# Optimization experiments

Measured on AMD Instinct MI355X. Metric: run time of the kernel, lower is better.

Reference implementation:

```python
import jax, jax.numpy as jnp
import numpy as np

E = 768
H_HEADS = 12


def trilinear_border_sample(feat_map, coords):
    """grid_sample 3D, mode='bilinear', padding_mode='border', align_corners=True.
    feat_map: (B, C, D, H, W); coords: (B, P, 3) in [-1,1], last dim = (x, y, z) -> (W, H, D).
    Returns (B, P, C).
    """
    B, C, D, H, W = feat_map.shape
    x, y, z = coords[..., 0], coords[..., 1], coords[..., 2]
    ix = (x + 1.0) * 0.5 * (W - 1)
    iy = (y + 1.0) * 0.5 * (H - 1)
    iz = (z + 1.0) * 0.5 * (D - 1)
    x0 = jnp.floor(ix); y0 = jnp.floor(iy); z0 = jnp.floor(iz)
    wx = ix - x0; wy = iy - y0; wz = iz - z0
    x0i = jnp.clip(x0, 0, W - 1).astype(jnp.int32)
    x1i = jnp.clip(x0 + 1, 0, W - 1).astype(jnp.int32)
    y0i = jnp.clip(y0, 0, H - 1).astype(jnp.int32)
    y1i = jnp.clip(y0 + 1, 0, H - 1).astype(jnp.int32)
    z0i = jnp.clip(z0, 0, D - 1).astype(jnp.int32)
    z1i = jnp.clip(z0 + 1, 0, D - 1).astype(jnp.int32)
    flat = feat_map.reshape(B, C, D * H * W)

    def gather(zi, yi, xi):
        idx = (zi * H + yi) * W + xi  # (B, P)
        return jnp.take_along_axis(flat, idx[:, None, :], axis=2)  # (B, C, P)

    out = (
        gather(z0i, y0i, x0i) * ((1 - wz) * (1 - wy) * (1 - wx))[:, None, :]
        + gather(z0i, y0i, x1i) * ((1 - wz) * (1 - wy) * wx)[:, None, :]
        + gather(z0i, y1i, x0i) * ((1 - wz) * wy * (1 - wx))[:, None, :]
        + gather(z0i, y1i, x1i) * ((1 - wz) * wy * wx)[:, None, :]
        + gather(z1i, y0i, x0i) * (wz * (1 - wy) * (1 - wx))[:, None, :]
        + gather(z1i, y0i, x1i) * (wz * (1 - wy) * wx)[:, None, :]
        + gather(z1i, y1i, x0i) * (wz * wy * (1 - wx))[:, None, :]
        + gather(z1i, y1i, x1i) * (wz * wy * wx)[:, None, :]
    )
    return out.transpose(0, 2, 1)  # (B, P, C)


def setup_inputs() -> dict:
    key = jax.random.key(0)
    ks = jax.random.split(key, 12)
    B, fullN, nb = 64, 513, 32
    s = 1.0 / np.sqrt(E)
    return {
        "x": jax.random.normal(ks[0], (B, fullN, E), jnp.float32),
        "bio_embed": jax.random.normal(ks[1], (B, E), jnp.float32),
        "base_coords": jax.random.uniform(ks[2], (nb, 3), jnp.float32),
        "offsets": jax.random.normal(ks[3], (B, nb, 3), jnp.float32) * 0.1,
        "confidence": jax.random.uniform(ks[4], (B, 1), jnp.float32),
        "sample_proj_w": jax.random.uniform(ks[5], (E, E), jnp.float32, -s, s),
        "sample_proj_b": jax.random.uniform(ks[6], (E,), jnp.float32, -s, s),
        "in_proj_w": jax.random.uniform(ks[7], (3 * E, E), jnp.float32, -s, s),
        "in_proj_b": jnp.zeros((3 * E,), jnp.float32),
        "out_proj_w": jax.random.uniform(ks[8], (E, E), jnp.float32, -s, s),
        "out_proj_b": jnp.zeros((E,), jnp.float32),
        "grid_size": 8,
    }


def reference(x, bio_embed, base_coords, offsets, confidence,
              sample_proj_w, sample_proj_b, in_proj_w, in_proj_b,
              out_proj_w, out_proj_b, grid_size):
    B, fullN, C = x.shape
    G = grid_size
    patch_tokens = x[:, 1:, :]  # (B, N, C), N = G^3
    feat_map = patch_tokens.transpose(0, 2, 1).reshape(B, C, G, G, G)

    coords = jnp.clip(base_coords[None, :, :] + offsets, -1.0, 1.0)  # (B, nb, 3)
    sampled = trilinear_border_sample(feat_map, coords)  # (B, nb, C)
    sampled = sampled @ sample_proj_w.T + sample_proj_b

    # MultiheadAttention: single query (bio_embed), keys/values = sampled tokens
    hd = E // H_HEADS
    Wq, Wk, Wv = in_proj_w[:E], in_proj_w[E:2 * E], in_proj_w[2 * E:]
    bq, bk, bv = in_proj_b[:E], in_proj_b[E:2 * E], in_proj_b[2 * E:]
    q = (bio_embed @ Wq.T + bq).reshape(B, H_HEADS, hd)
    k = (sampled @ Wk.T + bk).reshape(B, -1, H_HEADS, hd)
    v = (sampled @ Wv.T + bv).reshape(B, -1, H_HEADS, hd)
    scores = jnp.einsum('bhd,bphd->bhp', q, k) / jnp.sqrt(jnp.asarray(hd, q.dtype))
    attn = jax.nn.softmax(scores, axis=-1)
    ctx = jnp.einsum('bhp,bphd->bhd', attn, v).reshape(B, E)
    attn_out = ctx @ out_proj_w.T + out_proj_b  # (B, E)

    out = jnp.broadcast_to(attn_out[:, None, :], (B, fullN, C))
    out = out * confidence[:, :, None]
    return out
```

## Files before the change

kernel.cpp:

```cpp
#include <hip/hip_runtime.h>
#include <hip/hip_bf16.h>
#include <math.h>

#define E 768
#define NH 12
#define HD 64
#define NTHR 256

typedef __attribute__((ext_vector_type(8))) short bf16x8;
typedef __attribute__((ext_vector_type(4))) float f32x4;

__device__ __forceinline__ unsigned short f2bf_rne(float f) {
    unsigned int u = __float_as_uint(f);
    u += 0x7FFF + ((u >> 16) & 1);
    return (unsigned short)(u >> 16);
}

__device__ __forceinline__ float bf2f(unsigned short u) {
    return __uint_as_float((unsigned)u << 16);
}

__device__ __forceinline__ void sample_one(
    const float* x, const float* bcrd, const float* offs, int G,
    unsigned short* sampled, int u, int P, int fullN, int t, int tstep)
{
    int b = u / P, p = u % P;
    float gm1 = (float)(G - 1);

    float cx = bcrd[p * 3 + 0] + offs[u * 3 + 0];
    float cy = bcrd[p * 3 + 1] + offs[u * 3 + 1];
    float cz = bcrd[p * 3 + 2] + offs[u * 3 + 2];
    cx = fminf(fmaxf(cx, -1.f), 1.f);
    cy = fminf(fmaxf(cy, -1.f), 1.f);
    cz = fminf(fmaxf(cz, -1.f), 1.f);

    float ix = (cx + 1.f) * 0.5f * gm1;
    float iy = (cy + 1.f) * 0.5f * gm1;
    float iz = (cz + 1.f) * 0.5f * gm1;
    float fx = floorf(ix), fy = floorf(iy), fz = floorf(iz);
    float wx = ix - fx, wy = iy - fy, wz = iz - fz;

    int x0 = (int)fminf(fmaxf(fx,       0.f), gm1);
    int x1 = (int)fminf(fmaxf(fx + 1.f, 0.f), gm1);
    int y0 = (int)fminf(fmaxf(fy,       0.f), gm1);
    int y1 = (int)fminf(fmaxf(fy + 1.f, 0.f), gm1);
    int z0 = (int)fminf(fmaxf(fz,       0.f), gm1);
    int z1 = (int)fminf(fmaxf(fz + 1.f, 0.f), gm1);

    int tk[8];
    tk[0] = (z0 * G + y0) * G + x0;
    tk[1] = (z0 * G + y0) * G + x1;
    tk[2] = (z0 * G + y1) * G + x0;
    tk[3] = (z0 * G + y1) * G + x1;
    tk[4] = (z1 * G + y0) * G + x0;
    tk[5] = (z1 * G + y0) * G + x1;
    tk[6] = (z1 * G + y1) * G + x0;
    tk[7] = (z1 * G + y1) * G + x1;
    float wgt[8];
    wgt[0] = (1.f - wz) * (1.f - wy) * (1.f - wx);
    wgt[1] = (1.f - wz) * (1.f - wy) * wx;
    wgt[2] = (1.f - wz) * wy * (1.f - wx);
    wgt[3] = (1.f - wz) * wy * wx;
    wgt[4] = wz * (1.f - wy) * (1.f - wx);
    wgt[5] = wz * (1.f - wy) * wx;
    wgt[6] = wz * wy * (1.f - wx);
    wgt[7] = wz * wy * wx;

    const float4* xb4 = (const float4*)(x + ((size_t)b * fullN + 1) * E);
    ushort4* outp = (ushort4*)(sampled + (size_t)u * E);
    for (int c4 = t; c4 < E / 4; c4 += tstep) {
        float4 acc = {0.f, 0.f, 0.f, 0.f};
#pragma unroll
        for (int k = 0; k < 8; ++k) {
            float4 v = xb4[(size_t)tk[k] * (E / 4) + c4];
            acc.x += wgt[k] * v.x; acc.y += wgt[k] * v.y;
            acc.z += wgt[k] * v.z; acc.w += wgt[k] * v.w;
        }
        ushort4 o;
        o.x = f2bf_rne(acc.x); o.y = f2bf_rne(acc.y);
        o.z = f2bf_rne(acc.z); o.w = f2bf_rne(acc.w);
        outp[c4] = o;
    }
}

__device__ __forceinline__ void w2_tile(
    const float* Wkv, const float* spw, unsigned short* w2_bf,
    int n0, int k0, unsigned short* lsA, unsigned short* lsB)
{
    int t = threadIdx.x;
    int wv = t >> 6;
    int ln = t & 63;
    int wm = (wv & 1) * 32;
    int wn = (wv >> 1) * 32;

    f32x4 acc[2][2] = {};

    for (int j0 = 0; j0 < E; j0 += 32) {
#pragma unroll
        for (int rep = 0; rep < 2; ++rep) {
            int fi = t + rep * 256;
            int r = fi >> 3, c4 = fi & 7;
            float4 v = *(const float4*)(Wkv + (size_t)(n0 + r) * E + j0 + c4 * 4);
            ushort4 o;
            o.x = f2bf_rne(v.x); o.y = f2bf_rne(v.y);
            o.z = f2bf_rne(v.z); o.w = f2bf_rne(v.w);
            *(ushort4*)(lsA + r * 32 + c4 * 4) = o;
        }
        {
            int r = t >> 3, c8 = t & 7;
            const float* sp = spw + (size_t)(j0 + r) * E + k0 + c8 * 8;
            float4 v0 = *(const float4*)(sp);
            float4 v1 = *(const float4*)(sp + 4);
            int kb = c8 * 8;
            lsB[(kb + 0) * 32 + r] = f2bf_rne(v0.x);
            lsB[(kb + 1) * 32 + r] = f2bf_rne(v0.y);
            lsB[(kb + 2) * 32 + r] = f2bf_rne(v0.z);
            lsB[(kb + 3) * 32 + r] = f2bf_rne(v0.w);
            lsB[(kb + 4) * 32 + r] = f2bf_rne(v1.x);
            lsB[(kb + 5) * 32 + r] = f2bf_rne(v1.y);
            lsB[(kb + 6) * 32 + r] = f2bf_rne(v1.z);
            lsB[(kb + 7) * 32 + r] = f2bf_rne(v1.w);
        }
        __syncthreads();

        int kq = (ln >> 4) * 8;
        int rsel = ln & 15;
        bf16x8 af[2], bfr[2];
#pragma unroll
        for (int i = 0; i < 2; ++i) {
            af[i]  = *(const bf16x8*)&lsA[(wm + i * 16 + rsel) * 32 + kq];
            bfr[i] = *(const bf16x8*)&lsB[(wn + i * 16 + rsel) * 32 + kq];
        }
#pragma unroll
        for (int i = 0; i < 2; ++i)
#pragma unroll
            for (int j = 0; j < 2; ++j)
                acc[i][j] = __builtin_amdgcn_mfma_f32_16x16x32_bf16(
                    af[i], bfr[j], acc[i][j], 0, 0, 0);
        __syncthreads();
    }

    int cr = (ln >> 4) * 4;
    int cc = ln & 15;
#pragma unroll
    for (int j = 0; j < 2; ++j) {
        int col = k0 + wn + j * 16 + cc;
#pragma unroll
        for (int i = 0; i < 2; ++i) {
#pragma unroll
            for (int r = 0; r < 4; ++r) {
                int row = n0 + wm + i * 16 + cr + r;
                w2_bf[(size_t)row * E + col] = f2bf_rne(acc[i][j][r]);
            }
        }
    }
}

__device__ __forceinline__ void matvec_wave_v4(
    const float* A, const float* W, const float* bias, float* C,
    int u, int N, int ln)
{
    int m = u / N, n = u % N;
    const float4* a4 = (const float4*)(A + (size_t)m * E);
    const float4* w4 = (const float4*)(W + (size_t)n * E);
    float s = 0.f;
#pragma unroll
    for (int j = 0; j < 3; ++j) {
        float4 av = a4[ln + 64 * j];
        float4 wv = w4[ln + 64 * j];
        s += av.x * wv.x + av.y * wv.y + av.z * wv.z + av.w * wv.w;
    }
#pragma unroll
    for (int off = 32; off; off >>= 1) s += __shfl_down(s, off);
    if (ln == 0) C[u] = s + bias[n];
}

__global__ __launch_bounds__(256) void prep_kernel(
    const float* __restrict__ x,
    const float* __restrict__ bcrd, const float* __restrict__ offs,
    const int* __restrict__ gsize,
    const float* __restrict__ bio,
    const float* __restrict__ spw, const float* __restrict__ spb,
    const float* __restrict__ ipw, const float* __restrict__ ipb,
    const float* __restrict__ opb,
    unsigned short* __restrict__ sampled_bf, unsigned short* __restrict__ w2_bf,
    float* __restrict__ q, float* __restrict__ b2, float* __restrict__ aout,
    int B, int P, int fullN, int nb_sample, int nb_w2, int nb_q, int nb_b2)
{
    __shared__ unsigned short lsA[64 * 32];
    __shared__ unsigned short lsB[64 * 32];

    int blk = blockIdx.x;
    int t = threadIdx.x;
    int wv = t >> 6, ln = t & 63;
    const float* Wkv = ipw + (size_t)E * E;

    if (blk < nb_sample) {
        sample_one(x, bcrd, offs, *gsize, sampled_bf, blk, P, fullN, t, NTHR);
        return;
    }
    blk -= nb_sample;
    if (blk < nb_w2) {
        w2_tile(Wkv, spw, w2_bf, (blk / 12) * 64, (blk % 12) * 64, lsA, lsB);
        return;
    }
    blk -= nb_w2;
    if (blk < nb_q) {
        int u = blk * 4 + wv;
        if (u < B * E) matvec_wave_v4(bio, ipw, ipb, q, u, E, ln);
        return;
    }
    blk -= nb_q;
    if (blk < nb_b2) {
        int u = blk * 4 + wv;
        if (u < 2 * E) matvec_wave_v4(spb, Wkv, ipb + E, b2, u, 2 * E, ln);
        return;
    }
    blk -= nb_b2;
    {
        int i = blk * NTHR + t;
        float4 bb = ((const float4*)opb)[i % (E / 4)];
        ((float4*)aout)[i] = bb;
    }
}

__global__ __launch_bounds__(256) void attn_ctx_op(
    const float* __restrict__ q, const unsigned short* __restrict__ sampled_bf,
    const unsigned short* __restrict__ w2_bf, const float* __restrict__ b2,
    const float* __restrict__ opw, float* __restrict__ aout, int B, int P)
{
    __shared__ float q_lds[HD];
    __shared__ __align__(16) float u_lds[E];
    __shared__ float sc_lds[64];
    __shared__ float at_lds[64];
    __shared__ __align__(16) float cx_lds[E];
    __shared__ float ch_lds[HD];

    int b = blockIdx.x % B;
    int h = blockIdx.x / B;
    int t = threadIdx.x, wv = t >> 6, ln = t & 63;

    const unsigned short* W2k = w2_bf + (size_t)(h * HD) * E;
    const unsigned short* W2v = w2_bf + (size_t)(E + h * HD) * E;
    const unsigned short* smp = sampled_bf + (size_t)(b * P) * E;

    if (t < HD) q_lds[t] = q[(size_t)b * E + h * HD + t];
    __syncthreads();

    if (t < E / 4) {
        float4 uu = {0.f, 0.f, 0.f, 0.f};
        for (int d = 0; d < HD; ++d) {
            float qd = q_lds[d];
            ushort4 r = *(const ushort4*)(W2k + (size_t)d * E + 4 * t);
            uu.x += qd * bf2f(r.x); uu.y += qd * bf2f(r.y);
            uu.z += qd * bf2f(r.z); uu.w += qd * bf2f(r.w);
        }
        *(float4*)&u_lds[4 * t] = uu;
    }
    __syncthreads();

    for (int p = wv; p < P; p += 4) {
        const unsigned short* sr = smp + (size_t)p * E;
        float s = 0.f;
#pragma unroll
        for (int c = 0; c < E / 64; ++c)
            s += u_lds[ln + 64 * c] * bf2f(sr[ln + 64 * c]);
#pragma unroll
        for (int off = 32; off; off >>= 1) s += __shfl_xor(s, off);
        if (ln == 0) sc_lds[p] = s * 0.125f;
    }
    __syncthreads();

    if (wv == 0) {
        float s = (ln < P) ? sc_lds[ln] : -INFINITY;
        float mx = s;
#pragma unroll
        for (int off = 32; off; off >>= 1) mx = fmaxf(mx, __shfl_xor(mx, off));
        float ex = (ln < P) ? __expf(s - mx) : 0.f;
        float den = ex;
#pragma unroll
        for (int off = 32; off; off >>= 1) den += __shfl_xor(den, off);
        if (ln < P) at_lds[ln] = ex / den;
    }
    __syncthreads();

    if (t < E / 4) {
        float4 cc = {0.f, 0.f, 0.f, 0.f};
        for (int p = 0; p < P; ++p) {
            float a = at_lds[p];
            ushort4 r = *(const ushort4*)(smp + (size_t)p * E + 4 * t);
            cc.x += a * bf2f(r.x); cc.y += a * bf2f(r.y);
            cc.z += a * bf2f(r.z); cc.w += a * bf2f(r.w);
        }
        *(float4*)&cx_lds[4 * t] = cc;
    }
    __syncthreads();

    for (int d = wv; d < HD; d += 4) {
        const unsigned short* vr = W2v + (size_t)d * E;
        float s = 0.f;
#pragma unroll
        for (int c = 0; c < E / 64; ++c)
            s += cx_lds[ln + 64 * c] * bf2f(vr[ln + 64 * c]);
#pragma unroll
        for (int off = 32; off; off >>= 1) s += __shfl_down(s, off);
        if (ln == 0) ch_lds[d] = s + b2[E + h * HD + d];
    }
    __syncthreads();

#pragma unroll
    for (int jj = 0; jj < 3; ++jj) {
        int n = t + jj * NTHR;
        const float4* wr = (const float4*)(opw + (size_t)n * E + h * HD);
        float acc = 0.f;
#pragma unroll
        for (int c = 0; c < HD / 4; ++c) {
            float4 w = wr[c];
            acc += w.x * ch_lds[4 * c] + w.y * ch_lds[4 * c + 1]
                 + w.z * ch_lds[4 * c + 2] + w.w * ch_lds[4 * c + 3];
        }
        atomicAdd(&aout[(size_t)b * E + n], acc);
    }
}

__global__ void bcast_kernel(const float* __restrict__ attn_out,
                             const float* __restrict__ conf,
                             float* __restrict__ out,
                             int fullN, int pc)
{
    int b = blockIdx.y;
    float cf = conf[b];
    const float4* ao = (const float4*)(attn_out + (size_t)b * E);
    float4* ob = (float4*)(out + (size_t)b * fullN * E);
    int i = blockIdx.x * blockDim.x + threadIdx.x;
    if (i < pc) {
        int c4 = i % (E / 4);
        float4 v = ao[c4];
        v.x *= cf; v.y *= cf; v.z *= cf; v.w *= cf;
        ob[i] = v;
    }
}

extern "C" void kernel_launch(void* const* d_in, const int* in_sizes, int n_in,
                              void* d_out, int out_size, void* d_ws, size_t ws_size,
                              hipStream_t stream)
{
    const float* x      = (const float*)d_in[0];
    const float* bio    = (const float*)d_in[1];
    const float* bcrd   = (const float*)d_in[2];
    const float* offs   = (const float*)d_in[3];
    const float* conf   = (const float*)d_in[4];
    const float* spw    = (const float*)d_in[5];
    const float* spb    = (const float*)d_in[6];
    const float* ipw    = (const float*)d_in[7];
    const float* ipb    = (const float*)d_in[8];
    const float* opw    = (const float*)d_in[9];
    const float* opb    = (const float*)d_in[10];
    const int*   gsize  = (const int*)d_in[11];
    float* out = (float*)d_out;

    int B     = in_sizes[1] / E;
    int P     = in_sizes[2] / 3;
    int fullN = in_sizes[0] / (B * E);
    int M     = B * P;

    char* base = (char*)d_out;
    unsigned short* sampled_bf = (unsigned short*)(base + 0);
    unsigned short* w2_bf      = (unsigned short*)(base + 3145728);

    float* q    = (float*)d_ws;
    float* b2   = (float*)((char*)d_ws + 196608);
    float* aout = (float*)((char*)d_ws + 262144);

    int nb_sample = M;
    int nb_w2     = (2 * E / 64) * (E / 64);
    int nb_q      = (B * E + 3) / 4;
    int nb_b2     = (2 * E + 3) / 4;
    int nb_ai     = (B * E / 4) / NTHR;
    prep_kernel<<<nb_sample + nb_w2 + nb_q + nb_b2 + nb_ai, NTHR, 0, stream>>>(
        x, bcrd, offs, gsize, bio, spw, spb, ipw, ipb, opb,
        sampled_bf, w2_bf, q, b2, aout,
        B, P, fullN, nb_sample, nb_w2, nb_q, nb_b2);

    attn_ctx_op<<<B * NH, NTHR, 0, stream>>>(q, sampled_bf, w2_bf, b2,
                                             opw, aout, B, P);

    int pc = fullN * E / 4;
    bcast_kernel<<<dim3((pc + 255) / 256, B), NTHR, 0, stream>>>(
        aout, conf, out, fullN, pc);
}
```

Baseline: 261.2 us.

## Specialize attention loops for P=32 and rewrite broadcast with nontemporal row stores

Adds fully unrolled fast paths for the score and context loops when the number of sampled points is 32, and unrolls the q·Wk loop. The broadcast kernel is restructured so each 192-thread block loads the scaled attention vector once and writes 8 output rows with nontemporal stores. This drops the per-element modulo and repeated loads and aims to speed up the dominant output write, which is about 100MB. The cost is duplicated code paths and more register pressure from the unrolling.

```diff
diff --git a/kernel.cpp b/kernel.cpp
--- a/kernel.cpp
+++ b/kernel.cpp
@@ -249,6 +249,7 @@
 
     if (t < E / 4) {
         float4 uu = {0.f, 0.f, 0.f, 0.f};
+#pragma unroll
         for (int d = 0; d < HD; ++d) {
             float qd = q_lds[d];
             ushort4 r = *(const ushort4*)(W2k + (size_t)d * E + 4 * t);
@@ -259,15 +260,30 @@
     }
     __syncthreads();
 
-    for (int p = wv; p < P; p += 4) {
-        const unsigned short* sr = smp + (size_t)p * E;
-        float s = 0.f;
-#pragma unroll
-        for (int c = 0; c < E / 64; ++c)
-            s += u_lds[ln + 64 * c] * bf2f(sr[ln + 64 * c]);
-#pragma unroll
-        for (int off = 32; off; off >>= 1) s += __shfl_xor(s, off);
-        if (ln == 0) sc_lds[p] = s * 0.125f;
+    if (P == 32) {
+#pragma unroll
+        for (int pp = 0; pp < 8; ++pp) {
+            int p = wv + pp * 4;
+            const unsigned short* sr = smp + (size_t)p * E;
+            float s = 0.f;
+#pragma unroll
+            for (int c = 0; c < E / 64; ++c)
+                s += u_lds[ln + 64 * c] * bf2f(sr[ln + 64 * c]);
+#pragma unroll
+            for (int off = 32; off; off >>= 1) s += __shfl_xor(s, off);
+            if (ln == 0) sc_lds[p] = s * 0.125f;
+        }
+    } else {
+        for (int p = wv; p < P; p += 4) {
+            const unsigned short* sr = smp + (size_t)p * E;
+            float s = 0.f;
+#pragma unroll
+            for (int c = 0; c < E / 64; ++c)
+                s += u_lds[ln + 64 * c] * bf2f(sr[ln + 64 * c]);
+#pragma unroll
+            for (int off = 32; off; off >>= 1) s += __shfl_xor(s, off);
+            if (ln == 0) sc_lds[p] = s * 0.125f;
+        }
     }
     __syncthreads();
 
@@ -286,11 +302,21 @@
 
     if (t < E / 4) {
         float4 cc = {0.f, 0.f, 0.f, 0.f};
-        for (int p = 0; p < P; ++p) {
-            float a = at_lds[p];
-            ushort4 r = *(const ushort4*)(smp + (size_t)p * E + 4 * t);
-            cc.x += a * bf2f(r.x); cc.y += a * bf2f(r.y);
-            cc.z += a * bf2f(r.z); cc.w += a * bf2f(r.w);
+        if (P == 32) {
+#pragma unroll
+            for (int p = 0; p < 32; ++p) {
+                float a = at_lds[p];
+                ushort4 r = *(const ushort4*)(smp + (size_t)p * E + 4 * t);
+                cc.x += a * bf2f(r.x); cc.y += a * bf2f(r.y);
+                cc.z += a * bf2f(r.z); cc.w += a * bf2f(r.w);
+            }
+        } else {
+            for (int p = 0; p < P; ++p) {
+                float a = at_lds[p];
+                ushort4 r = *(const ushort4*)(smp + (size_t)p * E + 4 * t);
+                cc.x += a * bf2f(r.x); cc.y += a * bf2f(r.y);
+                cc.z += a * bf2f(r.z); cc.w += a * bf2f(r.w);
+            }
         }
         *(float4*)&cx_lds[4 * t] = cc;
     }
@@ -323,21 +349,24 @@
     }
 }
 
-__global__ void bcast_kernel(const float* __restrict__ attn_out,
-                             const float* __restrict__ conf,
-                             float* __restrict__ out,
-                             int fullN, int pc)
+#define ROWS_PER 8
+__global__ __launch_bounds__(192) void bcast_kernel(
+    const float* __restrict__ aout, const float* __restrict__ conf,
+    float* __restrict__ out, int fullN)
 {
     int b = blockIdx.y;
+    int t = threadIdx.x;
+    f32x4 v = ((const f32x4*)(aout + (size_t)b * E))[t];
     float cf = conf[b];
-    const float4* ao = (const float4*)(attn_out + (size_t)b * E);
-    float4* ob = (float4*)(out + (size_t)b * fullN * E);
-    int i = blockIdx.x * blockDim.x + threadIdx.x;
-    if (i < pc) {
-        int c4 = i % (E / 4);
-        float4 v = ao[c4];
-        v.x *= cf; v.y *= cf; v.z *= cf; v.w *= cf;
-        ob[i] = v;
+    v *= cf;
+
+    int r0 = blockIdx.x * ROWS_PER;
+    int nr = fullN - r0; if (nr > ROWS_PER) nr = ROWS_PER;
+    f32x4* ob = (f32x4*)(out + (size_t)b * fullN * E) + (size_t)r0 * (E / 4) + t;
+#pragma unroll
+    for (int r = 0; r < ROWS_PER; ++r) {
+        if (r < nr) __builtin_nontemporal_store(v, ob);
+        ob += E / 4;
     }
 }
 
@@ -385,7 +414,6 @@
     attn_ctx_op<<<B * NH, NTHR, 0, stream>>>(q, sampled_bf, w2_bf, b2,
                                              opw, aout, B, P);
 
-    int pc = fullN * E / 4;
-    bcast_kernel<<<dim3((pc + 255) / 256, B), NTHR, 0, stream>>>(
-        aout, conf, out, fullN, pc);
-}
+    bcast_kernel<<<dim3((fullN + ROWS_PER - 1) / ROWS_PER, B), 192, 0, stream>>>(
+        aout, conf, out, fullN);
+}
```

Result: no change. 262.0 us (+0.3%).
